# Optimization experiments

Measured on AMD Instinct MI355X. Metric: run time of the kernel, lower is better.

The kernel has to match this reference:

```python
import jax, jax.numpy as jnp
import numpy as np

B, S, H = 1, 2048, 1024   # batch, seq_len, hidden_size
E, K, I = 8, 2, 1024      # num_experts, top_k, intermediate_size


def setup_inputs() -> dict:
    key = jax.random.key(0)
    ks = jax.random.split(key, 5)
    x = jax.random.normal(ks[0], (B, S, H), dtype=jnp.float32)
    gate_w = jax.random.normal(ks[1], (H, E), dtype=jnp.float32) * 0.02
    wg = jax.random.normal(ks[2], (E, H, I), dtype=jnp.float32) * 0.02  # gate_proj per expert
    wu = jax.random.normal(ks[3], (E, H, I), dtype=jnp.float32) * 0.02  # up_proj per expert
    wd = jax.random.normal(ks[4], (E, I, H), dtype=jnp.float32) * 0.02  # down_proj per expert
    return {"x": x, "gate_w": gate_w, "wg": wg, "wu": wu, "wd": wd}


def _moe(x, gate_w, wg, wu, wd):
    b, s, h = x.shape
    n = b * s
    logits = jnp.einsum('bsh,he->bse', x, gate_w)          # [B,S,E]
    top_vals, sel = jax.lax.top_k(logits, K)               # [B,S,K]
    rweights = jax.nn.softmax(top_vals, axis=-1)           # [B,S,K]
    x_flat = x.reshape(n, h)
    sel_flat = sel.reshape(n, K)
    rw_flat = rweights.reshape(n, K)

    def expert_body(out, params):
        e, Wg, Wu, Wd = params
        hit = jnp.any(sel_flat == e, axis=-1)              # [N] tokens routed to e in any slot
        # stable argsort: hit tokens first, in ascending original index order
        perm = jnp.argsort(jnp.logical_not(hit))
        tokens = x_flat[perm]                              # [N,H] (row j = j-th token of token_indices)
        y = jnp.einsum('ni,ih->nh', jax.nn.silu(tokens @ Wg) * (tokens @ Wu), Wd)  # [N,H]
        contrib = jnp.zeros_like(out)
        for k in range(K):
            km = sel_flat[:, k] == e                       # [N]
            # original does output_flat[k_indices] += w * expert_output[:len(k_indices)]
            # i.e. j-th token of k_indices gets expert_output row j
            ranks = jnp.clip(jnp.cumsum(km) - 1, 0, n - 1)
            w = jnp.where(km, rw_flat[:, k], 0.0)
            contrib = contrib + w[:, None] * y[ranks]
        return out + contrib, None

    out, _ = jax.lax.scan(expert_body, jnp.zeros_like(x_flat),
                          (jnp.arange(E), wg, wu, wd))
    output = out.reshape(b, s, h)

    # aux metrics (match LoadBalancedRouter)
    probs = jax.nn.softmax(logits, axis=-1)
    usage = probs.mean(axis=(0, 1))                        # [E]
    balance_loss = jnp.var(usage, ddof=1) * E              # torch.var is unbiased
    su = jnp.sort(usage)
    idx = jnp.arange(1, E + 1, dtype=usage.dtype)
    gini = 2.0 * (idx * su).sum() / (E * su.sum()) - (E + 1.0) / E
    entropy = -(probs * jnp.log(probs + 1e-10)).sum(-1).mean()
    return output, balance_loss, gini, entropy


def reference(x, gate_w, wg, wu, wd):
    return _moe(x, gate_w, wg, wu, wd)
```

## Files before the change

kernel.cpp:

```cpp
#include <hip/hip_runtime.h>
#include <stdint.h>

#define TOKENS 2048
#define HID 1024
#define NE 8

typedef __attribute__((ext_vector_type(8))) short bf16x8;
typedef __attribute__((ext_vector_type(4))) float f32x4;

__device__ __forceinline__ unsigned short f2bf(float f) {
  unsigned int u = __float_as_uint(f);
  return (unsigned short)((u + 0x7fffu + ((u >> 16) & 1u)) >> 16);
}

__device__ __forceinline__ void gload16(const void* g, void* l) {
  __builtin_amdgcn_global_load_lds((const __attribute__((address_space(1))) void*)g,
                                   (__attribute__((address_space(3))) void*)l, 16, 0, 0);
}

__global__ __launch_bounds__(256) void k_pre(
    const float* __restrict__ x, const float* __restrict__ gw,
    const float* __restrict__ wg, const float* __restrict__ wu,
    unsigned short* __restrict__ wgt, unsigned short* __restrict__ wut,
    int* __restrict__ sel, float* __restrict__ rw,
    float* __restrict__ probs, float* __restrict__ ent) {
  __shared__ float tile[64][65];
  const int bid = blockIdx.x;
  const int tid = threadIdx.x;

  if (bid < 4096) {
    const int bx = bid & 15;
    const int by = (bid >> 4) & 15;
    const int e = (bid >> 8) & 7;
    const int tensor = (bid >> 11) & 1;
    const float* src = (tensor == 0 ? wg : wu) + ((size_t)e << 20);
    unsigned short* dst = (tensor == 0 ? wgt : wut) + ((size_t)e << 20);
    const int tr = tid >> 4, tc = (tid & 15) * 4;
#pragma unroll
    for (int p = 0; p < 4; ++p) {
      const int row = p * 16 + tr;
      const float4 v = *(const float4*)(src + (size_t)(by * 64 + row) * 1024 + bx * 64 + tc);
      tile[row][tc] = v.x; tile[row][tc + 1] = v.y; tile[row][tc + 2] = v.z; tile[row][tc + 3] = v.w;
    }
    __syncthreads();
#pragma unroll
    for (int p = 0; p < 4; ++p) {
      const int row = p * 16 + tr;
      const ushort4 o = make_ushort4(f2bf(tile[tc + 0][row]), f2bf(tile[tc + 1][row]),
                                     f2bf(tile[tc + 2][row]), f2bf(tile[tc + 3][row]));
      *(ushort4*)(dst + (size_t)(bx * 64 + row) * 1024 + by * 64 + tc) = o;
    }
    return;
  }

  const int w = tid >> 6;
  const int lane = tid & 63;
  const int t = (bid - 4096) * 4 + w;

  const float4* x4 = (const float4*)(x + (size_t)t * HID);
  const float4* gw4 = (const float4*)gw;

  float acc[NE];
#pragma unroll
  for (int e = 0; e < NE; ++e) acc[e] = 0.f;

#pragma unroll
  for (int i = 0; i < 4; ++i) {
    const int idx4 = i * 64 + lane;
    const float4 xv = x4[idx4];
    float4 g[8];
#pragma unroll
    for (int k = 0; k < 8; ++k) g[k] = gw4[(size_t)idx4 * 8 + k];
    const float xs[4] = {xv.x, xv.y, xv.z, xv.w};
#pragma unroll
    for (int c = 0; c < 4; ++c) {
      acc[0] += xs[c] * g[c * 2].x;
      acc[1] += xs[c] * g[c * 2].y;
      acc[2] += xs[c] * g[c * 2].z;
      acc[3] += xs[c] * g[c * 2].w;
      acc[4] += xs[c] * g[c * 2 + 1].x;
      acc[5] += xs[c] * g[c * 2 + 1].y;
      acc[6] += xs[c] * g[c * 2 + 1].z;
      acc[7] += xs[c] * g[c * 2 + 1].w;
    }
  }

#pragma unroll
  for (int e = 0; e < NE; ++e) {
#pragma unroll
    for (int msk = 32; msk >= 1; msk >>= 1) acc[e] += __shfl_xor(acc[e], msk, 64);
  }

  float mx = acc[0];
#pragma unroll
  for (int e = 1; e < NE; ++e) mx = fmaxf(mx, acc[e]);

  const int e8 = lane & 7;
  float my = acc[0];
#pragma unroll
  for (int k = 1; k < NE; ++k) if (e8 == k) my = acc[k];
  const float exl = expf(my - mx);
  float S = exl;
#pragma unroll
  for (int msk = 1; msk <= 4; msk <<= 1) S += __shfl_xor(S, msk, 64);
  const float pp = exl / S;
  if (lane < 8) probs[t * NE + lane] = pp;
  float ev = -pp * logf(pp + 1e-10f);
#pragma unroll
  for (int msk = 1; msk <= 4; msk <<= 1) ev += __shfl_xor(ev, msk, 64);

  if (lane == 0) {
    ent[t] = ev;
    int b0 = 0; float v0 = acc[0];
#pragma unroll
    for (int e = 1; e < NE; ++e) if (acc[e] > v0) { v0 = acc[e]; b0 = e; }
    int b1 = -1; float v1 = 0.f;
#pragma unroll
    for (int e = 0; e < NE; ++e) {
      if (e != b0 && (b1 < 0 || acc[e] > v1)) { v1 = acc[e]; b1 = e; }
    }
    const float w1e = expf(v1 - v0);
    const float s2 = 1.f + w1e;
    sel[t * 2] = b0; sel[t * 2 + 1] = b1;
    rw[t * 2] = 1.f / s2; rw[t * 2 + 1] = w1e / s2;
  }
}

__global__ void k_aux(const int* __restrict__ sel, int* __restrict__ cnt,
                      int* __restrict__ hit_list, int* __restrict__ rowidx,
                      const float* __restrict__ probs, const float* __restrict__ ent,
                      float* __restrict__ dout) {
  const int tid = threadIdx.x;

  if (blockIdx.x == 8) {
    __shared__ float red[256][NE];
    __shared__ float rede[256];
    const float4* p4 = (const float4*)probs;
    float pa[NE];
#pragma unroll
    for (int e = 0; e < NE; ++e) pa[e] = 0.f;
    float ea = 0.f;
    for (int t = tid; t < TOKENS; t += 256) {
      const float4 a = p4[t * 2];
      const float4 b = p4[t * 2 + 1];
      pa[0] += a.x; pa[1] += a.y; pa[2] += a.z; pa[3] += a.w;
      pa[4] += b.x; pa[5] += b.y; pa[6] += b.z; pa[7] += b.w;
      ea += ent[t];
    }
#pragma unroll
    for (int e = 0; e < NE; ++e) red[tid][e] = pa[e];
    rede[tid] = ea;
    __syncthreads();
    for (int s = 128; s >= 1; s >>= 1) {
      if (tid < s) {
#pragma unroll
        for (int e = 0; e < NE; ++e) red[tid][e] += red[tid + s][e];
        rede[tid] += rede[tid + s];
      }
      __syncthreads();
    }
    if (tid == 0) {
      float us[NE];
      for (int e = 0; e < NE; ++e) us[e] = red[0][e] / (float)TOKENS;
      float mean = 0.f;
      for (int e = 0; e < NE; ++e) mean += us[e];
      mean /= (float)NE;
      float var = 0.f;
      for (int e = 0; e < NE; ++e) { const float d = us[e] - mean; var += d * d; }
      var /= (float)(NE - 1);
      const float bl = var * (float)NE;
      for (int i = 1; i < NE; ++i) {
        const float key = us[i]; int j = i - 1;
        while (j >= 0 && us[j] > key) { us[j + 1] = us[j]; --j; }
        us[j + 1] = key;
      }
      float num = 0.f, den = 0.f;
      for (int i = 0; i < NE; ++i) { num += (float)(i + 1) * us[i]; den += us[i]; }
      const float gini = 2.f * num / ((float)NE * den) - (float)(NE + 1) / (float)NE;
      dout[(size_t)TOKENS * HID] = bl;
      dout[(size_t)TOKENS * HID + 1] = gini;
      dout[(size_t)TOKENS * HID + 2] = rede[0] / (float)TOKENS;
    }
    return;
  }

  const int e = blockIdx.x;
  __shared__ unsigned long long ssum[256];
  __shared__ unsigned long long csumA[256];
  __shared__ unsigned long long csumB[256];

  int s0[8], s1[8];
  unsigned long long mine = 0ull;
  unsigned long long cA = 0ull, cB = 0ull;
#pragma unroll
  for (int j = 0; j < 8; ++j) {
    const int t = tid * 8 + j;
    s0[j] = sel[2 * t]; s1[j] = sel[2 * t + 1];
#pragma unroll
    for (int q = 0; q < 4; ++q) {
      cA += ((unsigned long long)((s0[j] == q) + (s1[j] == q))) << (16 * q);
      cB += ((unsigned long long)((s0[j] == q + 4) + (s1[j] == q + 4))) << (16 * q);
    }
    const unsigned long long k0 = (s0[j] == e) ? 1ull : 0ull;
    const unsigned long long k1 = (s1[j] == e) ? 1ull : 0ull;
    mine += (k0 | k1) | (k0 << 21) | (k1 << 42);
  }
  ssum[tid] = mine;
  csumA[tid] = cA;
  csumB[tid] = cB;
  __syncthreads();
  for (int s = 128; s >= 1; s >>= 1) {
    if (tid < s) { csumA[tid] += csumA[tid + s]; csumB[tid] += csumB[tid + s]; }
    __syncthreads();
  }
  const unsigned long long totA = csumA[0];
  const unsigned long long totB = csumB[0];
  int tc[NE];
#pragma unroll
  for (int q = 0; q < 4; ++q) {
    tc[q] = (int)((totA >> (16 * q)) & 0xFFFFull);
    tc[q + 4] = (int)((totB >> (16 * q)) & 0xFFFFull);
  }
  if (e == 0 && tid < NE) cnt[tid] = tc[tid];
  int poff = 0;
#pragma unroll
  for (int q = 0; q < NE; ++q) if (q < e) poff += (tc[q] + 127) & ~127;

  for (int s = 1; s < 256; s <<= 1) {
    const unsigned long long v = (tid >= s) ? ssum[tid - s] : 0ull;
    __syncthreads();
    ssum[tid] += v;
    __syncthreads();
  }
  const unsigned long long excl = (tid > 0) ? ssum[tid - 1] : 0ull;
  int hc = (int)(excl & 0x1FFFFFull);
  int c0 = (int)((excl >> 21) & 0x1FFFFFull);
  int c1 = (int)((excl >> 42) & 0x1FFFFFull);
#pragma unroll
  for (int j = 0; j < 8; ++j) {
    const int t = tid * 8 + j;
    const int k0 = (s0[j] == e), k1 = (s1[j] == e);
    if (k0 | k1) { hit_list[poff + hc] = t; ++hc; }
    if (k0) { rowidx[2 * t] = poff + c0; ++c0; }
    if (k1) { rowidx[2 * t + 1] = poff + c1; ++c1; }
  }
}

__global__ void k_gather(const float* __restrict__ x, const int* __restrict__ hit_list,
                         const int* __restrict__ cnt, unsigned short* __restrict__ A) {
  const int mb = blockIdx.x, e = blockIdx.y;
  const int ce = cnt[e];
  const int pc = (ce + 127) & ~127;
  if (mb * 8 >= pc) return;
  int poff = 0;
  for (int q = 0; q < e; ++q) poff += (cnt[q] + 127) & ~127;
  const int tid = threadIdx.x;
#pragma unroll
  for (int i = 0; i < 8; ++i) {
    const int rr = mb * 8 + i;
    unsigned short* dst = A + (size_t)(poff + rr) * 1024 + tid * 4;
    if (rr < ce) {
      const int t = hit_list[poff + rr];
      const float4 v = *(const float4*)(x + (size_t)t * 1024 + tid * 4);
      *(ushort4*)dst = make_ushort4(f2bf(v.x), f2bf(v.y), f2bf(v.z), f2bf(v.w));
    } else {
      *(ushort4*)dst = make_ushort4(0, 0, 0, 0);
    }
  }
}

__global__ __launch_bounds__(256, 4) void k_gemm1(
    const unsigned short* __restrict__ A, const unsigned short* __restrict__ wgt,
    const unsigned short* __restrict__ wut, const int* __restrict__ cnt,
    unsigned short* __restrict__ T) {
  const int nb = blockIdx.x, mb = blockIdx.y, e = blockIdx.z;
  const int ce = cnt[e];
  if (mb * 128 >= ce) return;
  int poff = 0;
  for (int q = 0; q < e; ++q) poff += (cnt[q] + 127) & ~127;

  const unsigned short* Ab = A + (size_t)(poff + mb * 128) * 1024;
  const unsigned short* Bg = wgt + ((size_t)e << 20) + ((size_t)nb << 16);
  const unsigned short* Bu = wut + ((size_t)e << 20) + ((size_t)nb << 16);

  __shared__ __align__(16) short lds[3][8192];

  const int tid = threadIdx.x;
  const int lane = tid & 63;
  const int w = tid >> 6;
  const int wm = w & 1, wn = w >> 1;
  const int r = lane & 15, gq = lane >> 4;
  const int slot = gq ^ ((r >> 1) & 3);
  const int srow = lane >> 2;
  const int skoff = ((lane & 3) ^ ((lane >> 3) & 3)) << 3;

  f32x4 accg[4][2], accu[4][2];
  const f32x4 fz = {0.f, 0.f, 0.f, 0.f};
#pragma unroll
  for (int i = 0; i < 4; ++i)
#pragma unroll
    for (int j = 0; j < 2; ++j) { accg[i][j] = fz; accu[i][j] = fz; }

  auto stage = [&](int kt, int b) {
#pragma unroll
    for (int q = 0; q < 4; ++q) {
      const int gseg = w + q * 4;
      const unsigned short* sb;
      int seg;
      if (gseg < 8) { sb = Ab; seg = gseg; }
      else if (gseg < 12) { sb = Bg; seg = gseg - 8; }
      else { sb = Bu; seg = gseg - 12; }
      gload16(sb + (size_t)(seg * 16 + srow) * 1024 + kt * 32 + skoff,
              &lds[b][gseg * 512]);
    }
  };

  stage(0, 0); stage(1, 1); stage(2, 2);
  int curb = 0;
  for (int kt = 0; kt < 32; ++kt) {
    if (kt < 30)      { asm volatile("s_waitcnt vmcnt(8)" ::: "memory"); }
    else if (kt == 30){ asm volatile("s_waitcnt vmcnt(4)" ::: "memory"); }
    else              { asm volatile("s_waitcnt vmcnt(0)" ::: "memory"); }
    __builtin_amdgcn_sched_barrier(0);
    __builtin_amdgcn_s_barrier();
    __builtin_amdgcn_sched_barrier(0);

    const short* La = &lds[curb][0];
    const short* Lg = &lds[curb][4096];
    const short* Lu = &lds[curb][6144];
    bf16x8 af[4], gf[2], uf[2];
#pragma unroll
    for (int f = 0; f < 4; ++f)
      af[f] = *(const bf16x8*)(La + (wm * 64 + f * 16 + r) * 32 + slot * 8);
#pragma unroll
    for (int f = 0; f < 2; ++f) {
      gf[f] = *(const bf16x8*)(Lg + (wn * 32 + f * 16 + r) * 32 + slot * 8);
      uf[f] = *(const bf16x8*)(Lu + (wn * 32 + f * 16 + r) * 32 + slot * 8);
    }
    asm volatile("s_waitcnt lgkmcnt(0)" ::: "memory");
    __builtin_amdgcn_sched_barrier(0);
    __builtin_amdgcn_s_barrier();
    __builtin_amdgcn_sched_barrier(0);
    if (kt <= 28) stage(kt + 3, curb);

#pragma unroll
    for (int i = 0; i < 4; ++i)
#pragma unroll
      for (int j = 0; j < 2; ++j) {
        accg[i][j] = __builtin_amdgcn_mfma_f32_16x16x32_bf16(af[i], gf[j], accg[i][j], 0, 0, 0);
        accu[i][j] = __builtin_amdgcn_mfma_f32_16x16x32_bf16(af[i], uf[j], accu[i][j], 0, 0, 0);
      }
    curb = (curb == 2) ? 0 : curb + 1;
  }

  const size_t rowbase = (size_t)(poff + mb * 128);
#pragma unroll
  for (int i = 0; i < 4; ++i)
#pragma unroll
    for (int j = 0; j < 2; ++j) {
      const int col = nb * 64 + wn * 32 + j * 16 + r;
#pragma unroll
      for (int rr = 0; rr < 4; ++rr) {
        const int rowt = wm * 64 + i * 16 + gq * 4 + rr;
        const float gv = accg[i][j][rr];
        const float uv = accu[i][j][rr];
        const float sv = gv / (1.f + expf(-gv)) * uv;
        T[(rowbase + rowt) * 1024 + col] = f2bf(sv);
      }
    }
}

__global__ __launch_bounds__(256, 4) void k_gemm2(
    const unsigned short* __restrict__ T, const float* __restrict__ wd,
    const int* __restrict__ cnt, float* __restrict__ Y) {
  const int nb = blockIdx.x, mb = blockIdx.y, e = blockIdx.z;
  const int ce = cnt[e];
  if (mb * 128 >= ce) return;
  int poff = 0;
  for (int q = 0; q < e; ++q) poff += (cnt[q] + 127) & ~127;

  const unsigned short* Ab = T + (size_t)(poff + mb * 128) * 1024;
  const float* Wd = wd + ((size_t)e << 20) + nb * 64;

  __shared__ __align__(16) short lds[3][6144];

  const int tid = threadIdx.x;
  const int lane = tid & 63;
  const int w = tid >> 6;
  const int wm = w & 1, wn = w >> 1;
  const int r = lane & 15, gq = lane >> 4;
  const int aslot = gq ^ ((r >> 1) & 3);
  const int srow = lane >> 2;
  const int skoff = ((lane & 3) ^ ((lane >> 3) & 3)) << 3;
  const int wn_ = tid & 63, wkoct = tid >> 6;
  const int wps = wkoct ^ ((wn_ >> 1) & 3);

  f32x4 acc[4][2];
  const f32x4 fz = {0.f, 0.f, 0.f, 0.f};
#pragma unroll
  for (int i = 0; i < 4; ++i)
#pragma unroll
    for (int j = 0; j < 2; ++j) acc[i][j] = fz;

  auto stageA = [&](int kt, int b) {
#pragma unroll
    for (int q = 0; q < 2; ++q) {
      const int seg = w + q * 4;
      gload16(Ab + (size_t)(seg * 16 + srow) * 1024 + kt * 32 + skoff,
              &lds[b][seg * 512]);
    }
  };
  auto wload = [&](int kt, float* f) {
    const float* s = Wd + (size_t)(kt * 32 + wkoct * 8) * 1024 + wn_;
#pragma unroll
    for (int i = 0; i < 8; ++i) f[i] = s[i * 1024];
  };
  auto wwrite = [&](int b, const float* f) {
    unsigned int pk[4];
#pragma unroll
    for (int j = 0; j < 4; ++j)
      asm("v_cvt_pk_bf16_f32 %0, %1, %2" : "=v"(pk[j]) : "v"(f[2 * j]), "v"(f[2 * j + 1]));
    *(uint4*)((char*)&lds[b][4096] + wn_ * 64 + wps * 16) =
        make_uint4(pk[0], pk[1], pk[2], pk[3]);
  };

  stageA(0, 0); stageA(1, 1); stageA(2, 2);
  float dA[8], dB[8];
  wload(0, dA);
  wload(1, dB);
  wwrite(0, dA);
  wload(2, dA);
  wwrite(1, dB);
  asm volatile("s_waitcnt lgkmcnt(0)" ::: "memory");

  auto iter = [&](int kt, float* l, const float* s) {
    asm volatile("s_waitcnt vmcnt(20)" ::: "memory");
    __builtin_amdgcn_sched_barrier(0);
    __builtin_amdgcn_s_barrier();
    __builtin_amdgcn_sched_barrier(0);
    const int curb = kt % 3;
    const short* La = &lds[curb][0];
    const short* Lb = &lds[curb][4096];
    bf16x8 af[4], bfr[2];
#pragma unroll
    for (int f = 0; f < 4; ++f)
      af[f] = *(const bf16x8*)(La + (wm * 64 + f * 16 + r) * 32 + aslot * 8);
#pragma unroll
    for (int f = 0; f < 2; ++f)
      bfr[f] = *(const bf16x8*)(Lb + (wn * 32 + f * 16 + r) * 32 + aslot * 8);
    asm volatile("s_waitcnt lgkmcnt(0)" ::: "memory");
    __builtin_amdgcn_sched_barrier(0);
    __builtin_amdgcn_s_barrier();
    __builtin_amdgcn_sched_barrier(0);
    if (kt <= 28) {
      wload(kt + 3, l);
      stageA(kt + 3, curb);
    }
#pragma unroll
    for (int i = 0; i < 4; ++i)
#pragma unroll
      for (int j = 0; j < 2; ++j)
        acc[i][j] = __builtin_amdgcn_mfma_f32_16x16x32_bf16(af[i], bfr[j], acc[i][j], 0, 0, 0);
    if (kt <= 29) wwrite((kt + 2) % 3, s);
  };

  for (int k2 = 0; k2 < 15; ++k2) {
    iter(2 * k2,     dB, dA);
    iter(2 * k2 + 1, dA, dB);
  }
#pragma unroll
  for (int kt = 30; kt < 32; ++kt) {
    if (kt == 30) { asm volatile("s_waitcnt vmcnt(10)" ::: "memory"); }
    else          { asm volatile("s_waitcnt vmcnt(0)" ::: "memory"); }
    __builtin_amdgcn_sched_barrier(0);
    __builtin_amdgcn_s_barrier();
    __builtin_amdgcn_sched_barrier(0);
    const int curb = kt % 3;
    const short* La = &lds[curb][0];
    const short* Lb = &lds[curb][4096];
    bf16x8 af[4], bfr[2];
#pragma unroll
    for (int f = 0; f < 4; ++f)
      af[f] = *(const bf16x8*)(La + (wm * 64 + f * 16 + r) * 32 + aslot * 8);
#pragma unroll
    for (int f = 0; f < 2; ++f)
      bfr[f] = *(const bf16x8*)(Lb + (wn * 32 + f * 16 + r) * 32 + aslot * 8);
    asm volatile("s_waitcnt lgkmcnt(0)" ::: "memory");
    __builtin_amdgcn_sched_barrier(0);
    __builtin_amdgcn_s_barrier();
    __builtin_amdgcn_sched_barrier(0);
#pragma unroll
    for (int i = 0; i < 4; ++i)
#pragma unroll
      for (int j = 0; j < 2; ++j)
        acc[i][j] = __builtin_amdgcn_mfma_f32_16x16x32_bf16(af[i], bfr[j], acc[i][j], 0, 0, 0);
  }

  const size_t rowbase = (size_t)(poff + mb * 128);
#pragma unroll
  for (int i = 0; i < 4; ++i)
#pragma unroll
    for (int j = 0; j < 2; ++j) {
      const int col = nb * 64 + wn * 32 + j * 16 + r;
#pragma unroll
      for (int rr = 0; rr < 4; ++rr) {
        const int rowt = wm * 64 + i * 16 + gq * 4 + rr;
        Y[(rowbase + rowt) * 1024 + col] = acc[i][j][rr];
      }
    }
}

__global__ void k_out(const float* __restrict__ Y, const int* __restrict__ rowidx,
                      const float* __restrict__ rw, float* __restrict__ out) {
  const int t = blockIdx.x;
  const int tid = threadIdx.x;
  const int r0 = rowidx[2 * t], r1 = rowidx[2 * t + 1];
  const float w0 = rw[2 * t], w1 = rw[2 * t + 1];
  const float4 y0 = *(const float4*)(Y + (size_t)r0 * HID + tid * 4);
  const float4 y1 = *(const float4*)(Y + (size_t)r1 * HID + tid * 4);
  float4 o;
  o.x = w0 * y0.x + w1 * y1.x;
  o.y = w0 * y0.y + w1 * y1.y;
  o.z = w0 * y0.z + w1 * y1.z;
  o.w = w0 * y0.w + w1 * y1.w;
  *(float4*)(out + (size_t)t * HID + tid * 4) = o;
}

extern "C" void kernel_launch(void* const* d_in, const int* in_sizes, int n_in,
                              void* d_out, int out_size, void* d_ws, size_t ws_size,
                              hipStream_t stream) {
  const float* x = (const float*)d_in[0];
  const float* gw = (const float*)d_in[1];
  const float* wg = (const float*)d_in[2];
  const float* wu = (const float*)d_in[3];
  const float* wd = (const float*)d_in[4];
  float* out = (float*)d_out;

  char* p = (char*)d_ws;
  unsigned short* wgt = (unsigned short*)p;
  unsigned short* wut = (unsigned short*)(p + 16777216);
  float* Y = (float*)p;
  unsigned short* A = (unsigned short*)(p + 33554432);
  unsigned short* T = (unsigned short*)(p + 46137344);
  char* q = p + 58720256;
  float* probs = (float*)q; q += 65536;
  float* ent = (float*)q; q += 8192;
  int* sel = (int*)q; q += 16384;
  float* rwp = (float*)q; q += 16384;
  int* rowidx = (int*)q; q += 16384;
  int* hit_list = (int*)q; q += 20480;
  int* cnt = (int*)q;

  k_pre<<<4608, 256, 0, stream>>>(x, gw, wg, wu, wgt, wut, sel, rwp, probs, ent);
  k_aux<<<9, 256, 0, stream>>>(sel, cnt, hit_list, rowidx, probs, ent, out);
  k_gather<<<dim3(256, 8), 256, 0, stream>>>(x, hit_list, cnt, A);
  k_gemm1<<<dim3(16, 16, 8), 256, 0, stream>>>(A, wgt, wut, cnt, T);
  k_gemm2<<<dim3(16, 16, 8), 256, 0, stream>>>(T, wd, cnt, Y);
  k_out<<<2048, 256, 0, stream>>>(Y, rowidx, rwp, out);
}
```

Baseline: 122.3 us.

## Swap which weights are pre-transposed: fuse fp32 gate/up conversion into gemm1, pretranspose down

The pre-pass now transposes and converts only the down-projection weights to bf16, instead of both the gate and up weights. gemm1 loads fp32 gate/up weights directly from global memory, converts them in registers and writes them into swizzled LDS. gemm2 uses the pre-transposed bf16 down weights through direct global-to-LDS loads. This halves the pre-pass transpose traffic (8M elements instead of 16M). In exchange gemm1 moves twice as many fp32 weight bytes per tile, does in-register conversion, and has its occupancy hint lowered from 4 to 3.

```diff
diff --git a/kernel.cpp b/kernel.cpp
--- a/kernel.cpp
+++ b/kernel.cpp
@@ -20,21 +20,19 @@
 
 __global__ __launch_bounds__(256) void k_pre(
     const float* __restrict__ x, const float* __restrict__ gw,
-    const float* __restrict__ wg, const float* __restrict__ wu,
-    unsigned short* __restrict__ wgt, unsigned short* __restrict__ wut,
+    const float* __restrict__ wd, unsigned short* __restrict__ wdt,
     int* __restrict__ sel, float* __restrict__ rw,
     float* __restrict__ probs, float* __restrict__ ent) {
   __shared__ float tile[64][65];
   const int bid = blockIdx.x;
   const int tid = threadIdx.x;
 
-  if (bid < 4096) {
+  if (bid < 2048) {
     const int bx = bid & 15;
     const int by = (bid >> 4) & 15;
-    const int e = (bid >> 8) & 7;
-    const int tensor = (bid >> 11) & 1;
-    const float* src = (tensor == 0 ? wg : wu) + ((size_t)e << 20);
-    unsigned short* dst = (tensor == 0 ? wgt : wut) + ((size_t)e << 20);
+    const int e = bid >> 8;
+    const float* src = wd + ((size_t)e << 20);
+    unsigned short* dst = wdt + ((size_t)e << 20);
     const int tr = tid >> 4, tc = (tid & 15) * 4;
 #pragma unroll
     for (int p = 0; p < 4; ++p) {
@@ -55,7 +53,7 @@
 
   const int w = tid >> 6;
   const int lane = tid & 63;
-  const int t = (bid - 4096) * 4 + w;
+  const int t = (bid - 2048) * 4 + w;
 
   const float4* x4 = (const float4*)(x + (size_t)t * HID);
   const float4* gw4 = (const float4*)gw;
@@ -269,9 +267,9 @@
   }
 }
 
-__global__ __launch_bounds__(256, 4) void k_gemm1(
-    const unsigned short* __restrict__ A, const unsigned short* __restrict__ wgt,
-    const unsigned short* __restrict__ wut, const int* __restrict__ cnt,
+__global__ __launch_bounds__(256, 3) void k_gemm1(
+    const unsigned short* __restrict__ A, const float* __restrict__ wg,
+    const float* __restrict__ wu, const int* __restrict__ cnt,
     unsigned short* __restrict__ T) {
   const int nb = blockIdx.x, mb = blockIdx.y, e = blockIdx.z;
   const int ce = cnt[e];
@@ -280,10 +278,174 @@
   for (int q = 0; q < e; ++q) poff += (cnt[q] + 127) & ~127;
 
   const unsigned short* Ab = A + (size_t)(poff + mb * 128) * 1024;
-  const unsigned short* Bg = wgt + ((size_t)e << 20) + ((size_t)nb << 16);
-  const unsigned short* Bu = wut + ((size_t)e << 20) + ((size_t)nb << 16);
+  const float* Wg = wg + ((size_t)e << 20) + nb * 64;
+  const float* Wu = wu + ((size_t)e << 20) + nb * 64;
 
   __shared__ __align__(16) short lds[3][8192];
+
+  const int tid = threadIdx.x;
+  const int lane = tid & 63;
+  const int w = tid >> 6;
+  const int wm = w & 1, wn = w >> 1;
+  const int r = lane & 15, gq = lane >> 4;
+  const int aslot = gq ^ ((r >> 1) & 3);
+  const int wslot = gq ^ ((r >> 2) & 3);
+  const int srow = lane >> 2;
+  const int skoff = ((lane & 3) ^ ((lane >> 3) & 3)) << 3;
+  const int kp = tid >> 4, n4i = tid & 15;
+
+  f32x4 accg[4][2], accu[4][2];
+  const f32x4 fz = {0.f, 0.f, 0.f, 0.f};
+#pragma unroll
+  for (int i = 0; i < 4; ++i)
+#pragma unroll
+    for (int j = 0; j < 2; ++j) { accg[i][j] = fz; accu[i][j] = fz; }
+
+  auto stageA = [&](int kt, int b) {
+#pragma unroll
+    for (int q = 0; q < 2; ++q) {
+      const int seg = w + q * 4;
+      gload16(Ab + (size_t)(seg * 16 + srow) * 1024 + kt * 32 + skoff,
+              &lds[b][seg * 512]);
+    }
+  };
+  auto wload = [&](const float* W, int kt, float4& r0, float4& r1) {
+    const float* s = W + (size_t)(kt * 32 + 2 * kp) * 1024 + 4 * n4i;
+    r0 = *(const float4*)s;
+    r1 = *(const float4*)(s + 1024);
+  };
+  auto wwrite = [&](int b, int base, const float4& lo, const float4& hi) {
+    short* Lw = &lds[b][base];
+    const float l4[4] = {lo.x, lo.y, lo.z, lo.w};
+    const float h4[4] = {hi.x, hi.y, hi.z, hi.w};
+#pragma unroll
+    for (int j = 0; j < 4; ++j) {
+      unsigned int pk;
+      asm("v_cvt_pk_bf16_f32 %0, %1, %2" : "=v"(pk) : "v"(l4[j]), "v"(h4[j]));
+      const int n = 4 * n4i + j;
+      const int ps = (kp >> 2) ^ (n4i & 3);
+      *(unsigned int*)(Lw + n * 32 + ps * 8 + (kp & 3) * 2) = pk;
+    }
+  };
+
+  stageA(0, 0); stageA(1, 1); stageA(2, 2);
+  float4 g0A, g1A, u0A, u1A, g0B, g1B, u0B, u1B;
+  wload(Wg, 0, g0A, g1A); wload(Wu, 0, u0A, u1A);
+  wload(Wg, 1, g0B, g1B); wload(Wu, 1, u0B, u1B);
+  wwrite(0, 4096, g0A, g1A); wwrite(0, 6144, u0A, u1A);
+  wload(Wg, 2, g0A, g1A); wload(Wu, 2, u0A, u1A);
+  wwrite(1, 4096, g0B, g1B); wwrite(1, 6144, u0B, u1B);
+  asm volatile("s_waitcnt lgkmcnt(0)" ::: "memory");
+
+  auto iter = [&](int kt, float4& lg0, float4& lg1, float4& lu0, float4& lu1,
+                  const float4& sg0, const float4& sg1, const float4& su0, const float4& su1) {
+    asm volatile("s_waitcnt vmcnt(12)" ::: "memory");
+    __builtin_amdgcn_sched_barrier(0);
+    __builtin_amdgcn_s_barrier();
+    __builtin_amdgcn_sched_barrier(0);
+    const int curb = kt % 3;
+    const short* La = &lds[curb][0];
+    const short* Lg = &lds[curb][4096];
+    const short* Lu = &lds[curb][6144];
+    bf16x8 af[4], gf[2], uf[2];
+#pragma unroll
+    for (int f = 0; f < 4; ++f)
+      af[f] = *(const bf16x8*)(La + (wm * 64 + f * 16 + r) * 32 + aslot * 8);
+#pragma unroll
+    for (int f = 0; f < 2; ++f) {
+      gf[f] = *(const bf16x8*)(Lg + (wn * 32 + f * 16 + r) * 32 + wslot * 8);
+      uf[f] = *(const bf16x8*)(Lu + (wn * 32 + f * 16 + r) * 32 + wslot * 8);
+    }
+    asm volatile("s_waitcnt lgkmcnt(0)" ::: "memory");
+    __builtin_amdgcn_sched_barrier(0);
+    __builtin_amdgcn_s_barrier();
+    __builtin_amdgcn_sched_barrier(0);
+    if (kt <= 28) {
+      wload(Wg, kt + 3, lg0, lg1);
+      wload(Wu, kt + 3, lu0, lu1);
+      stageA(kt + 3, curb);
+    }
+    if (kt <= 29) {
+      const int wb = (kt + 2) % 3;
+      wwrite(wb, 4096, sg0, sg1);
+      wwrite(wb, 6144, su0, su1);
+    }
+#pragma unroll
+    for (int i = 0; i < 4; ++i)
+#pragma unroll
+      for (int j = 0; j < 2; ++j) {
+        accg[i][j] = __builtin_amdgcn_mfma_f32_16x16x32_bf16(af[i], gf[j], accg[i][j], 0, 0, 0);
+        accu[i][j] = __builtin_amdgcn_mfma_f32_16x16x32_bf16(af[i], uf[j], accu[i][j], 0, 0, 0);
+      }
+  };
+
+  for (int k2 = 0; k2 < 15; ++k2) {
+    iter(2 * k2,     g0B, g1B, u0B, u1B, g0A, g1A, u0A, u1A);
+    iter(2 * k2 + 1, g0A, g1A, u0A, u1A, g0B, g1B, u0B, u1B);
+  }
+#pragma unroll
+  for (int kt = 30; kt < 32; ++kt) {
+    if (kt == 30) { asm volatile("s_waitcnt vmcnt(6)" ::: "memory"); }
+    else          { asm volatile("s_waitcnt vmcnt(0)" ::: "memory"); }
+    __builtin_amdgcn_sched_barrier(0);
+    __builtin_amdgcn_s_barrier();
+    __builtin_amdgcn_sched_barrier(0);
+    const int curb = kt % 3;
+    const short* La = &lds[curb][0];
+    const short* Lg = &lds[curb][4096];
+    const short* Lu = &lds[curb][6144];
+    bf16x8 af[4], gf[2], uf[2];
+#pragma unroll
+    for (int f = 0; f < 4; ++f)
+      af[f] = *(const bf16x8*)(La + (wm * 64 + f * 16 + r) * 32 + aslot * 8);
+#pragma unroll
+    for (int f = 0; f < 2; ++f) {
+      gf[f] = *(const bf16x8*)(Lg + (wn * 32 + f * 16 + r) * 32 + wslot * 8);
+      uf[f] = *(const bf16x8*)(Lu + (wn * 32 + f * 16 + r) * 32 + wslot * 8);
+    }
+    asm volatile("s_waitcnt lgkmcnt(0)" ::: "memory");
+    __builtin_amdgcn_sched_barrier(0);
+    __builtin_amdgcn_s_barrier();
+    __builtin_amdgcn_sched_barrier(0);
+#pragma unroll
+    for (int i = 0; i < 4; ++i)
+#pragma unroll
+      for (int j = 0; j < 2; ++j) {
+        accg[i][j] = __builtin_amdgcn_mfma_f32_16x16x32_bf16(af[i], gf[j], accg[i][j], 0, 0, 0);
+        accu[i][j] = __builtin_amdgcn_mfma_f32_16x16x32_bf16(af[i], uf[j], accu[i][j], 0, 0, 0);
+      }
+  }
+
+  const size_t rowbase = (size_t)(poff + mb * 128);
+#pragma unroll
+  for (int i = 0; i < 4; ++i)
+#pragma unroll
+    for (int j = 0; j < 2; ++j) {
+      const int col = nb * 64 + wn * 32 + j * 16 + r;
+#pragma unroll
+      for (int rr = 0; rr < 4; ++rr) {
+        const int rowt = wm * 64 + i * 16 + gq * 4 + rr;
+        const float gv = accg[i][j][rr];
+        const float uv = accu[i][j][rr];
+        const float sv = gv / (1.f + expf(-gv)) * uv;
+        T[(rowbase + rowt) * 1024 + col] = f2bf(sv);
+      }
+    }
+}
+
+__global__ __launch_bounds__(256, 4) void k_gemm2(
+    const unsigned short* __restrict__ T, const unsigned short* __restrict__ wdt,
+    const int* __restrict__ cnt, float* __restrict__ Y) {
+  const int nb = blockIdx.x, mb = blockIdx.y, e = blockIdx.z;
+  const int ce = cnt[e];
+  if (mb * 128 >= ce) return;
+  int poff = 0;
+  for (int q = 0; q < e; ++q) poff += (cnt[q] + 127) & ~127;
+
+  const unsigned short* Ab = T + (size_t)(poff + mb * 128) * 1024;
+  const unsigned short* Bd = wdt + ((size_t)e << 20) + ((size_t)nb << 16);
+
+  __shared__ __align__(16) short lds[3][6144];
 
   const int tid = threadIdx.x;
   const int lane = tid & 63;
@@ -294,22 +456,21 @@
   const int srow = lane >> 2;
   const int skoff = ((lane & 3) ^ ((lane >> 3) & 3)) << 3;
 
-  f32x4 accg[4][2], accu[4][2];
+  f32x4 acc[4][2];
   const f32x4 fz = {0.f, 0.f, 0.f, 0.f};
 #pragma unroll
   for (int i = 0; i < 4; ++i)
 #pragma unroll
-    for (int j = 0; j < 2; ++j) { accg[i][j] = fz; accu[i][j] = fz; }
+    for (int j = 0; j < 2; ++j) acc[i][j] = fz;
 
   auto stage = [&](int kt, int b) {
 #pragma unroll
-    for (int q = 0; q < 4; ++q) {
+    for (int q = 0; q < 3; ++q) {
       const int gseg = w + q * 4;
       const unsigned short* sb;
       int seg;
       if (gseg < 8) { sb = Ab; seg = gseg; }
-      else if (gseg < 12) { sb = Bg; seg = gseg - 8; }
-      else { sb = Bu; seg = gseg - 12; }
+      else { sb = Bd; seg = gseg - 8; }
       gload16(sb + (size_t)(seg * 16 + srow) * 1024 + kt * 32 + skoff,
               &lds[b][gseg * 512]);
     }
@@ -318,182 +479,34 @@
   stage(0, 0); stage(1, 1); stage(2, 2);
   int curb = 0;
   for (int kt = 0; kt < 32; ++kt) {
-    if (kt < 30)      { asm volatile("s_waitcnt vmcnt(8)" ::: "memory"); }
-    else if (kt == 30){ asm volatile("s_waitcnt vmcnt(4)" ::: "memory"); }
+    if (kt < 30)      { asm volatile("s_waitcnt vmcnt(6)" ::: "memory"); }
+    else if (kt == 30){ asm volatile("s_waitcnt vmcnt(3)" ::: "memory"); }
     else              { asm volatile("s_waitcnt vmcnt(0)" ::: "memory"); }
     __builtin_amdgcn_sched_barrier(0);
     __builtin_amdgcn_s_barrier();
     __builtin_amdgcn_sched_barrier(0);
 
-    const short* La = &lds[curb][0];
-    const short* Lg = &lds[curb][4096];
-    const short* Lu = &lds[curb][6144];
-    bf16x8 af[4], gf[2], uf[2];
-#pragma unroll
-    for (int f = 0; f < 4; ++f)
-      af[f] = *(const bf16x8*)(La + (wm * 64 + f * 16 + r) * 32 + slot * 8);
-#pragma unroll
-    for (int f = 0; f < 2; ++f) {
-      gf[f] = *(const bf16x8*)(Lg + (wn * 32 + f * 16 + r) * 32 + slot * 8);
-      uf[f] = *(const bf16x8*)(Lu + (wn * 32 + f * 16 + r) * 32 + slot * 8);
-    }
-    asm volatile("s_waitcnt lgkmcnt(0)" ::: "memory");
-    __builtin_amdgcn_sched_barrier(0);
-    __builtin_amdgcn_s_barrier();
-    __builtin_amdgcn_sched_barrier(0);
-    if (kt <= 28) stage(kt + 3, curb);
-
-#pragma unroll
-    for (int i = 0; i < 4; ++i)
-#pragma unroll
-      for (int j = 0; j < 2; ++j) {
-        accg[i][j] = __builtin_amdgcn_mfma_f32_16x16x32_bf16(af[i], gf[j], accg[i][j], 0, 0, 0);
-        accu[i][j] = __builtin_amdgcn_mfma_f32_16x16x32_bf16(af[i], uf[j], accu[i][j], 0, 0, 0);
-      }
-    curb = (curb == 2) ? 0 : curb + 1;
-  }
-
-  const size_t rowbase = (size_t)(poff + mb * 128);
-#pragma unroll
-  for (int i = 0; i < 4; ++i)
-#pragma unroll
-    for (int j = 0; j < 2; ++j) {
-      const int col = nb * 64 + wn * 32 + j * 16 + r;
-#pragma unroll
-      for (int rr = 0; rr < 4; ++rr) {
-        const int rowt = wm * 64 + i * 16 + gq * 4 + rr;
-        const float gv = accg[i][j][rr];
-        const float uv = accu[i][j][rr];
-        const float sv = gv / (1.f + expf(-gv)) * uv;
-        T[(rowbase + rowt) * 1024 + col] = f2bf(sv);
-      }
-    }
-}
-
-__global__ __launch_bounds__(256, 4) void k_gemm2(
-    const unsigned short* __restrict__ T, const float* __restrict__ wd,
-    const int* __restrict__ cnt, float* __restrict__ Y) {
-  const int nb = blockIdx.x, mb = blockIdx.y, e = blockIdx.z;
-  const int ce = cnt[e];
-  if (mb * 128 >= ce) return;
-  int poff = 0;
-  for (int q = 0; q < e; ++q) poff += (cnt[q] + 127) & ~127;
-
-  const unsigned short* Ab = T + (size_t)(poff + mb * 128) * 1024;
-  const float* Wd = wd + ((size_t)e << 20) + nb * 64;
-
-  __shared__ __align__(16) short lds[3][6144];
-
-  const int tid = threadIdx.x;
-  const int lane = tid & 63;
-  const int w = tid >> 6;
-  const int wm = w & 1, wn = w >> 1;
-  const int r = lane & 15, gq = lane >> 4;
-  const int aslot = gq ^ ((r >> 1) & 3);
-  const int srow = lane >> 2;
-  const int skoff = ((lane & 3) ^ ((lane >> 3) & 3)) << 3;
-  const int wn_ = tid & 63, wkoct = tid >> 6;
-  const int wps = wkoct ^ ((wn_ >> 1) & 3);
-
-  f32x4 acc[4][2];
-  const f32x4 fz = {0.f, 0.f, 0.f, 0.f};
-#pragma unroll
-  for (int i = 0; i < 4; ++i)
-#pragma unroll
-    for (int j = 0; j < 2; ++j) acc[i][j] = fz;
-
-  auto stageA = [&](int kt, int b) {
-#pragma unroll
-    for (int q = 0; q < 2; ++q) {
-      const int seg = w + q * 4;
-      gload16(Ab + (size_t)(seg * 16 + srow) * 1024 + kt * 32 + skoff,
-              &lds[b][seg * 512]);
-    }
-  };
-  auto wload = [&](int kt, float* f) {
-    const float* s = Wd + (size_t)(kt * 32 + wkoct * 8) * 1024 + wn_;
-#pragma unroll
-    for (int i = 0; i < 8; ++i) f[i] = s[i * 1024];
-  };
-  auto wwrite = [&](int b, const float* f) {
-    unsigned int pk[4];
-#pragma unroll
-    for (int j = 0; j < 4; ++j)
-      asm("v_cvt_pk_bf16_f32 %0, %1, %2" : "=v"(pk[j]) : "v"(f[2 * j]), "v"(f[2 * j + 1]));
-    *(uint4*)((char*)&lds[b][4096] + wn_ * 64 + wps * 16) =
-        make_uint4(pk[0], pk[1], pk[2], pk[3]);
-  };
-
-  stageA(0, 0); stageA(1, 1); stageA(2, 2);
-  float dA[8], dB[8];
-  wload(0, dA);
-  wload(1, dB);
-  wwrite(0, dA);
-  wload(2, dA);
-  wwrite(1, dB);
-  asm volatile("s_waitcnt lgkmcnt(0)" ::: "memory");
-
-  auto iter = [&](int kt, float* l, const float* s) {
-    asm volatile("s_waitcnt vmcnt(20)" ::: "memory");
-    __builtin_amdgcn_sched_barrier(0);
-    __builtin_amdgcn_s_barrier();
-    __builtin_amdgcn_sched_barrier(0);
-    const int curb = kt % 3;
     const short* La = &lds[curb][0];
     const short* Lb = &lds[curb][4096];
     bf16x8 af[4], bfr[2];
 #pragma unroll
     for (int f = 0; f < 4; ++f)
-      af[f] = *(const bf16x8*)(La + (wm * 64 + f * 16 + r) * 32 + aslot * 8);
+      af[f] = *(const bf16x8*)(La + (wm * 64 + f * 16 + r) * 32 + slot * 8);
 #pragma unroll
     for (int f = 0; f < 2; ++f)
-      bfr[f] = *(const bf16x8*)(Lb + (wn * 32 + f * 16 + r) * 32 + aslot * 8);
+      bfr[f] = *(const bf16x8*)(Lb + (wn * 32 + f * 16 + r) * 32 + slot * 8);
     asm volatile("s_waitcnt lgkmcnt(0)" ::: "memory");
     __builtin_amdgcn_sched_barrier(0);
     __builtin_amdgcn_s_barrier();
     __builtin_amdgcn_sched_barrier(0);
-    if (kt <= 28) {
-      wload(kt + 3, l);
-      stageA(kt + 3, curb);
-    }
+    if (kt <= 28) stage(kt + 3, curb);
+
 #pragma unroll
     for (int i = 0; i < 4; ++i)
 #pragma unroll
       for (int j = 0; j < 2; ++j)
         acc[i][j] = __builtin_amdgcn_mfma_f32_16x16x32_bf16(af[i], bfr[j], acc[i][j], 0, 0, 0);
-    if (kt <= 29) wwrite((kt + 2) % 3, s);
-  };
-
-  for (int k2 = 0; k2 < 15; ++k2) {
-    iter(2 * k2,     dB, dA);
-    iter(2 * k2 + 1, dA, dB);
-  }
-#pragma unroll
-  for (int kt = 30; kt < 32; ++kt) {
-    if (kt == 30) { asm volatile("s_waitcnt vmcnt(10)" ::: "memory"); }
-    else          { asm volatile("s_waitcnt vmcnt(0)" ::: "memory"); }
-    __builtin_amdgcn_sched_barrier(0);
-    __builtin_amdgcn_s_barrier();
-    __builtin_amdgcn_sched_barrier(0);
-    const int curb = kt % 3;
-    const short* La = &lds[curb][0];
-    const short* Lb = &lds[curb][4096];
-    bf16x8 af[4], bfr[2];
-#pragma unroll
-    for (int f = 0; f < 4; ++f)
-      af[f] = *(const bf16x8*)(La + (wm * 64 + f * 16 + r) * 32 + aslot * 8);
-#pragma unroll
-    for (int f = 0; f < 2; ++f)
-      bfr[f] = *(const bf16x8*)(Lb + (wn * 32 + f * 16 + r) * 32 + aslot * 8);
-    asm volatile("s_waitcnt lgkmcnt(0)" ::: "memory");
-    __builtin_amdgcn_sched_barrier(0);
-    __builtin_amdgcn_s_barrier();
-    __builtin_amdgcn_sched_barrier(0);
-#pragma unroll
-    for (int i = 0; i < 4; ++i)
-#pragma unroll
-      for (int j = 0; j < 2; ++j)
-        acc[i][j] = __builtin_amdgcn_mfma_f32_16x16x32_bf16(af[i], bfr[j], acc[i][j], 0, 0, 0);
+    curb = (curb == 2) ? 0 : curb + 1;
   }
 
   const size_t rowbase = (size_t)(poff + mb * 128);
@@ -537,12 +550,11 @@
   float* out = (float*)d_out;
 
   char* p = (char*)d_ws;
-  unsigned short* wgt = (unsigned short*)p;
-  unsigned short* wut = (unsigned short*)(p + 16777216);
-  float* Y = (float*)p;
-  unsigned short* A = (unsigned short*)(p + 33554432);
-  unsigned short* T = (unsigned short*)(p + 46137344);
-  char* q = p + 58720256;
+  unsigned short* wdt = (unsigned short*)p;
+  unsigned short* A = (unsigned short*)(p + 16777216);
+  unsigned short* T = (unsigned short*)(p + 29360128);
+  float* Y = (float*)(p + 41943040);
+  char* q = p + 65011712;
   float* probs = (float*)q; q += 65536;
   float* ent = (float*)q; q += 8192;
   int* sel = (int*)q; q += 16384;
@@ -551,10 +563,10 @@
   int* hit_list = (int*)q; q += 20480;
   int* cnt = (int*)q;
 
-  k_pre<<<4608, 256, 0, stream>>>(x, gw, wg, wu, wgt, wut, sel, rwp, probs, ent);
+  k_pre<<<2560, 256, 0, stream>>>(x, gw, wd, wdt, sel, rwp, probs, ent);
   k_aux<<<9, 256, 0, stream>>>(sel, cnt, hit_list, rowidx, probs, ent, out);
   k_gather<<<dim3(256, 8), 256, 0, stream>>>(x, hit_list, cnt, A);
-  k_gemm1<<<dim3(16, 16, 8), 256, 0, stream>>>(A, wgt, wut, cnt, T);
-  k_gemm2<<<dim3(16, 16, 8), 256, 0, stream>>>(T, wd, cnt, Y);
+  k_gemm1<<<dim3(16, 16, 8), 256, 0, stream>>>(A, wg, wu, cnt, T);
+  k_gemm2<<<dim3(16, 16, 8), 256, 0, stream>>>(T, wdt, cnt, Y);
   k_out<<<2048, 256, 0, stream>>>(Y, rowidx, rwp, out);
 }
```

Measured after the change: 115.9 us. 1.06x faster.
